# Performance work log

Hardware: AMD Instinct MI355X
Metric: run time of the kernel (lower is better)

Reference implementation:

```python
import jax, jax.numpy as jnp
import numpy as np

B, T, D, HD, HN, O = 32, 512, 512, 64, 16, 512
EPS = 1e-5


def setup_inputs() -> dict:
    key = jax.random.key(0)
    ks = jax.random.split(key, 12)
    s = lambda fan_in: 1.0 / np.sqrt(fan_in)
    inp = {
        "inputs": jax.random.normal(ks[0], (B, T, D), dtype=jnp.float32),
        "Wq": jax.random.uniform(ks[1], (HN, D, HD), jnp.float32, -s(D), s(D)),
        "bq": jnp.zeros((HN, HD), jnp.float32),
        "Wk": jax.random.uniform(ks[2], (HN, D, HD), jnp.float32, -s(D), s(D)),
        "bk": jnp.zeros((HN, HD), jnp.float32),
        "Wv": jax.random.uniform(ks[3], (HN, D, HD), jnp.float32, -s(D), s(D)),
        "bv": jnp.zeros((HN, HD), jnp.float32),
        "Wr": jax.random.uniform(ks[4], (D, O), jnp.float32, -s(D), s(D)),
        "br": jnp.zeros((O,), jnp.float32),
        "Wo": jax.random.uniform(ks[5], (HN * HD, O), jnp.float32, -s(HN * HD), s(HN * HD)),
        "bo": jnp.zeros((O,), jnp.float32),
        "ln1_w": jnp.ones((O,), jnp.float32),
        "ln1_b": jnp.zeros((O,), jnp.float32),
        "Wfc": jax.random.uniform(ks[6], (O, O), jnp.float32, -s(O), s(O)),
        "bfc": jnp.zeros((O,), jnp.float32),
        "ln2_w": jnp.ones((O,), jnp.float32),
        "ln2_b": jnp.zeros((O,), jnp.float32),
    }
    return inp


def _layernorm(x, w, b):
    mu = jnp.mean(x, axis=-1, keepdims=True)
    var = jnp.mean(jnp.square(x - mu), axis=-1, keepdims=True)
    return (x - mu) * jax.lax.rsqrt(var + EPS) * w + b


def reference(inputs, Wq, bq, Wk, bk, Wv, bv, Wr, br, Wo, bo,
              ln1_w, ln1_b, Wfc, bfc, ln2_w, ln2_b):
    # causal mask: multiply-then-subtract as in the original
    score_mask = jnp.tril(jnp.ones((T, T), jnp.float32))        # [T,T]
    padding_mask = (score_mask == 0).astype(jnp.float32) * 1e9  # [T,T]

    residual = inputs @ Wr + br                                  # [B,T,O]

    # batched per-head projections with nonstandard activations
    q = jax.nn.relu(jnp.einsum('btd,hdf->bhtf', inputs, Wq) + bq[None, :, None, :])
    k = jax.nn.relu(jnp.einsum('btd,hdf->bhtf', inputs, Wk) + bk[None, :, None, :])
    v = jnp.tanh(jnp.einsum('btd,hdf->bhtf', inputs, Wv) + bv[None, :, None, :])

    scores = jnp.einsum('bhtf,bhsf->bhts', q, k) / jnp.sqrt(jnp.float32(HD))
    scores = scores * score_mask - padding_mask                  # [B,H,T,T]
    weights = jax.nn.softmax(scores, axis=-1)
    heads = jnp.einsum('bhts,bhsf->bhtf', weights, v)            # [B,H,T,HD]

    # concat heads (head order preserved) + tanh output projection
    concat = heads.transpose(0, 2, 1, 3).reshape(B, T, HN * HD)
    out = jnp.tanh(concat @ Wo + bo)                             # [B,T,O]

    out = _layernorm(out + residual, ln1_w, ln1_b)
    fc = jax.nn.relu(out @ Wfc + bfc)
    out = _layernorm(fc + out, ln2_w, ln2_b)
    return out
```

## Files before the change

### kernel.cpp

```cpp
#include <hip/hip_runtime.h>
#include <hip/hip_bf16.h>

#define B_  32
#define T_  512
#define D_  512
#define HD_ 64
#define HN_ 16
#define O_  512
#define M_  (B_ * T_)
#define NQ_ (HN_ * HD_)

typedef __bf16 bf16;
typedef __attribute__((ext_vector_type(8))) __bf16 bf16x8;
typedef __attribute__((ext_vector_type(4))) __bf16 bf16x4;
typedef __attribute__((ext_vector_type(4))) float f32x4;

static __device__ __forceinline__ f32x4 mfma16(bf16x8 a, bf16x8 b, f32x4 c) {
    return __builtin_amdgcn_mfma_f32_16x16x32_bf16(a, b, c, 0, 0, 0);
}

static __device__ __forceinline__ void load_lds_16B(const bf16* g, bf16* l) {
    __builtin_amdgcn_global_load_lds(
        (const __attribute__((address_space(1))) unsigned int*)(unsigned long long)g,
        (__attribute__((address_space(3))) unsigned int*)(unsigned long long)l,
        16, 0, 0);
}

static __device__ __forceinline__ float fast_tanh(float x) {
    return 1.f - 2.f / (__expf(2.f * x) + 1.f);
}

static __device__ __forceinline__ int2 swz_block() {
    const int nx = gridDim.x;
    const int nwg = nx * gridDim.y;
    int l = blockIdx.y * nx + blockIdx.x;
    l = (l & 7) * (nwg >> 3) + (l >> 3);
    return make_int2(l % nx, l / nx);
}

__global__ __launch_bounds__(256) void prep_headw_kernel(
    const float* __restrict__ Wq, const float* __restrict__ Wk,
    const float* __restrict__ Wv, bf16* __restrict__ wall)
{
    __shared__ bf16 tl[64][72];
    int id = blockIdx.x;
    const int kt = id & 7; id >>= 3;
    const int h = id & 15; id >>= 4;
    const float* src = (id == 0) ? Wq : (id == 1) ? Wk : Wv;
    bf16* dst = wall + (size_t)id * (1024 * 512);
    const int tid = threadIdx.x;
    const int k0 = kt * 64;
#pragma unroll
    for (int i = 0; i < 4; i++) {
        const int e = i * 256 + tid;
        const int kk = e >> 4, f4 = (e & 15) * 4;
        const f32x4 v = *(const f32x4*)(src + ((size_t)h * 512 + k0 + kk) * 64 + f4);
#pragma unroll
        for (int j = 0; j < 4; j++) tl[f4 + j][kk] = (bf16)v[j];
    }
    __syncthreads();
#pragma unroll
    for (int i = 0; i < 2; i++) {
        const int e = i * 256 + tid;
        const int f = e >> 3, kc = (e & 7) * 8;
        *(bf16x8*)(dst + ((size_t)h * 64 + f) * 512 + k0 + kc) = *(const bf16x8*)&tl[f][kc];
    }
}

__global__ __launch_bounds__(256) void prep_plain_kernel(
    const float* __restrict__ Wr, const float* __restrict__ Wo,
    const float* __restrict__ Wfc,
    bf16* __restrict__ wrt, bf16* __restrict__ wot, bf16* __restrict__ wfct)
{
    __shared__ bf16 tl[64][72];
    int id = blockIdx.x;
    const float* src; bf16* dst; int K;
    if (id < 64)       { src = Wr;  dst = wrt;  K = 512;  }
    else if (id < 192) { src = Wo;  dst = wot;  K = 1024; id -= 64; }
    else               { src = Wfc; dst = wfct; K = 512;  id -= 192; }
    const int kt = id >> 3, nt = id & 7;
    const int k0 = kt * 64, n0 = nt * 64;
    const int tid = threadIdx.x;
#pragma unroll
    for (int i = 0; i < 4; i++) {
        const int e = i * 256 + tid;
        const int kk = e >> 4, n4 = (e & 15) * 4;
        const f32x4 v = *(const f32x4*)(src + (size_t)(k0 + kk) * 512 + n0 + n4);
#pragma unroll
        for (int j = 0; j < 4; j++) tl[n4 + j][kk] = (bf16)v[j];
    }
    __syncthreads();
#pragma unroll
    for (int i = 0; i < 2; i++) {
        const int e = i * 256 + tid;
        const int nn = e >> 3, kc = (e & 7) * 8;
        *(bf16x8*)(dst + (size_t)(n0 + nn) * K + k0 + kc) = *(const bf16x8*)&tl[nn][kc];
    }
}

__global__ __launch_bounds__(256) void conv_input_kernel(
    const float* __restrict__ in, bf16* __restrict__ out)
{
    const size_t i = ((size_t)blockIdx.x * 256 + threadIdx.x) * 8;
    f32x4 x0 = *(const f32x4*)(in + i);
    f32x4 x1 = *(const f32x4*)(in + i + 4);
    bf16x8 v;
    v[0] = (bf16)x0[0]; v[1] = (bf16)x0[1]; v[2] = (bf16)x0[2]; v[3] = (bf16)x0[3];
    v[4] = (bf16)x1[0]; v[5] = (bf16)x1[1]; v[6] = (bf16)x1[2]; v[7] = (bf16)x1[3];
    *(bf16x8*)(out + i) = v;
}

__global__ __launch_bounds__(256) void pack_bias_kernel(
    const float* __restrict__ bq, const float* __restrict__ bk,
    const float* __restrict__ bv, const float* __restrict__ br,
    float* __restrict__ ball)
{
    const int i = blockIdx.x * 256 + threadIdx.x;
    float v = (i < 1024) ? bq[i]
            : (i < 2048) ? bk[i - 1024]
            : (i < 3072) ? bv[i - 2048] : br[i - 3072];
    ball[i] = v;
}

__device__ __forceinline__ void gemm_mainloop_db(
    const bf16* __restrict__ A, const bf16* __restrict__ Wt,
    const int K, const int m0, const int n0, const int tid,
    bf16 (*As)[128 * 64], bf16 (*Bs)[128 * 64], f32x4 (&acc)[4][4])
{
    const int lane = tid & 63;
    const int w = tid >> 6;
    const int wr = w >> 1, wc = w & 1;
    const int lr = lane & 15, lg = lane >> 4;
    const int nt = K >> 6;

    auto STAGE = [&](int buf, int k0) {
#pragma unroll
        for (int i = 0; i < 4; i++) {
            const int p = i * 256 + tid;
            const int row = p >> 3;
            const int g = (p & 7) ^ (row & 7);
            load_lds_16B(A + (size_t)(m0 + row) * K + k0 + g * 8, As[buf] + p * 8);
            load_lds_16B(Wt + (size_t)(n0 + row) * K + k0 + g * 8, Bs[buf] + p * 8);
        }
    };

    STAGE(0, 0);
    asm volatile("s_waitcnt vmcnt(0)\n\ts_barrier" ::: "memory");

    for (int t = 0; t < nt; t++) {
        const int cur = t & 1;
        if (t + 1 < nt) STAGE(cur ^ 1, (t + 1) << 6);
#pragma unroll
        for (int kc = 0; kc < 2; kc++) {
            bf16x8 a[4], b[4];
#pragma unroll
            for (int mi = 0; mi < 4; mi++) {
                const int row = wr * 64 + mi * 16 + lr;
                a[mi] = *(const bf16x8*)&As[cur][row * 64 + ((((kc << 2) | lg) ^ (row & 7)) << 3)];
            }
#pragma unroll
            for (int nj = 0; nj < 4; nj++) {
                const int row = wc * 64 + nj * 16 + lr;
                b[nj] = *(const bf16x8*)&Bs[cur][row * 64 + ((((kc << 2) | lg) ^ (row & 7)) << 3)];
            }
#pragma unroll
            for (int mi = 0; mi < 4; mi++)
#pragma unroll
                for (int nj = 0; nj < 4; nj++)
                    acc[mi][nj] = mfma16(a[mi], b[nj], acc[mi][nj]);
        }
        asm volatile("s_waitcnt vmcnt(0)\n\ts_barrier" ::: "memory");
    }
}

__global__ __launch_bounds__(256) void gemm_qkvr_kernel(
    const bf16* __restrict__ A, const bf16* __restrict__ Wall,
    const float* __restrict__ ball,
    bf16* __restrict__ qc, bf16* __restrict__ kb, bf16* __restrict__ vt,
    bf16* __restrict__ resb)
{
    __shared__ bf16 As[2][128 * 64];
    __shared__ bf16 Bs[2][128 * 64];
    const int tid = threadIdx.x;
    const int2 bc = swz_block();
    const int m0 = bc.y * 128, n0 = bc.x * 128;
    f32x4 acc[4][4];
    const f32x4 zero4 = {0.f, 0.f, 0.f, 0.f};
#pragma unroll
    for (int i = 0; i < 4; i++)
#pragma unroll
        for (int j = 0; j < 4; j++) acc[i][j] = zero4;

    gemm_mainloop_db(A, Wall, 512, m0, n0, tid, As, Bs, acc);

    const int lane = tid & 63, w = tid >> 6;
    const int wr = w >> 1, wc = w & 1, lr = lane & 15, lg = lane >> 4;
    const int region = n0 >> 10;
#pragma unroll
    for (int mi = 0; mi < 4; mi++) {
#pragma unroll
        for (int nj = 0; nj < 4; nj++) {
            const int n = n0 + wc * 64 + nj * 16 + lr;
            const float bn = ball[n];
            if (region == 2) {
                const int m = m0 + wr * 64 + mi * 16 + lg * 4;
                const int bb = m >> 9, t = m & 511;
                const int nn = n - 2048, hh = nn >> 6, f = nn & 63;
                bf16x4 st;
#pragma unroll
                for (int r = 0; r < 4; r++) st[r] = (bf16)fast_tanh(acc[mi][nj][r] + bn);
                *(bf16x4*)(vt + (((size_t)(bb * 16 + hh) * 64 + f) << 9) + t) = st;
            } else if (region == 3) {
                const int nn = n - 3072;
#pragma unroll
                for (int r = 0; r < 4; r++) {
                    const int m = m0 + wr * 64 + mi * 16 + lg * 4 + r;
                    resb[(size_t)m * 512 + nn] = (bf16)(acc[mi][nj][r] + bn);
                }
            } else {
                bf16* dst = region ? kb : qc;
                const int nn = n & 1023;
#pragma unroll
                for (int r = 0; r < 4; r++) {
                    const int m = m0 + wr * 64 + mi * 16 + lg * 4 + r;
                    dst[(size_t)m * 1024 + nn] = (bf16)fmaxf(acc[mi][nj][r] + bn, 0.f);
                }
            }
        }
    }
}

template <int ACT>
__global__ __launch_bounds__(256) void gemm_std_kernel(
    const bf16* __restrict__ A, const bf16* __restrict__ Wt,
    const float* __restrict__ bias, bf16* __restrict__ C, const int K)
{
    __shared__ bf16 As[2][128 * 64];
    __shared__ bf16 Bs[2][128 * 64];
    const int tid = threadIdx.x;
    const int2 bc = swz_block();
    const int m0 = bc.y * 128, n0 = bc.x * 128;
    f32x4 acc[4][4];
    const f32x4 zero4 = {0.f, 0.f, 0.f, 0.f};
#pragma unroll
    for (int i = 0; i < 4; i++)
#pragma unroll
        for (int j = 0; j < 4; j++) acc[i][j] = zero4;

    gemm_mainloop_db(A, Wt, K, m0, n0, tid, As, Bs, acc);

    const int lane = tid & 63, w = tid >> 6;
    const int wr = w >> 1, wc = w & 1, lr = lane & 15, lg = lane >> 4;
#pragma unroll
    for (int mi = 0; mi < 4; mi++) {
#pragma unroll
        for (int nj = 0; nj < 4; nj++) {
            const int n = n0 + wc * 64 + nj * 16 + lr;
            const float bn = bias[n];
#pragma unroll
            for (int r = 0; r < 4; r++) {
                const int m = m0 + wr * 64 + mi * 16 + lg * 4 + r;
                float v = acc[mi][nj][r] + bn;
                if constexpr (ACT == 1) v = fmaxf(v, 0.f);
                else if constexpr (ACT == 2) v = fast_tanh(v);
                C[(size_t)m * 512 + n] = (bf16)v;
            }
        }
    }
}

static __device__ __forceinline__ int sigma_k(int t) {
    return (t & 32) | ((t & 4) << 2) | ((t & 24) >> 1) | (t & 3);
}

__global__ __launch_bounds__(256) void mfma_attn_kernel(
    const bf16* __restrict__ Kb, const bf16* __restrict__ Vt, bf16* __restrict__ QC)
{
    __shared__ bf16 Ks[2][64][72];
    __shared__ bf16 Vts[2][64][72];

    int l = blockIdx.x;
    l = (l & 7) * 256 + (l >> 3);
    const int qb = l & 3;
    const int h = (l >> 2) & 15;
    const int b = l >> 6;
    const int tid = threadIdx.x;
    const int lane = tid & 63;
    const int w = tid >> 6;
    const int lr = lane & 15, lg = lane >> 4;

    const int qrow0 = qb * 128 + w * 32;
    const size_t qbase = ((size_t)b * T_ + qrow0) * NQ_ + h * 64;
    const int bh = b * HN_ + h;

    bf16x8 qf[2][2];
#pragma unroll
    for (int mi = 0; mi < 2; mi++)
#pragma unroll
        for (int kc = 0; kc < 2; kc++)
            qf[mi][kc] = *(const bf16x8*)(QC + qbase + (size_t)(mi * 16 + lr) * NQ_ + kc * 32 + lg * 8);

    const f32x4 zero4 = {0.f, 0.f, 0.f, 0.f};
    f32x4 o[2][4];
    float m_st[2] = {-1e30f, -1e30f}, l_st[2] = {0.f, 0.f};
#pragma unroll
    for (int mi = 0; mi < 2; mi++)
#pragma unroll
        for (int dj = 0; dj < 4; dj++) o[mi][dj] = zero4;

    const int nsb = 2 * qb + 2;

    bf16x8 kreg[2], vreg[2];
    auto LOADR = [&](int sb) {
#pragma unroll
        for (int i = 0; i < 2; i++) {
            const int ci = i * 256 + tid, row = ci >> 3, cc = ci & 7;
            kreg[i] = *(const bf16x8*)(Kb + ((size_t)b * T_ + sb * 64 + row) * NQ_ + h * 64 + cc * 8);
            vreg[i] = *(const bf16x8*)(Vt + ((size_t)bh * 64 + row) * T_ + sb * 64 + cc * 8);
        }
    };
    auto WRITE = [&](int buf) {
#pragma unroll
        for (int i = 0; i < 2; i++) {
            const int ci = i * 256 + tid, row = ci >> 3, cc = ci & 7;
            *(bf16x8*)&Ks[buf][sigma_k(row)][cc * 8] = kreg[i];
            *(bf16x8*)&Vts[buf][row][cc * 8] = vreg[i];
        }
    };

    LOADR(0); WRITE(0); __syncthreads();
    int cur = 0;

    for (int sb = 0; sb < nsb; sb++) {
        const bool pf = (sb + 1 < nsb);
        if (pf) LOADR(sb + 1);

        if (sb * 64 <= qrow0 + 31) {
            f32x4 sc[2][4];
#pragma unroll
            for (int mi = 0; mi < 2; mi++)
#pragma unroll
                for (int nj = 0; nj < 4; nj++) sc[mi][nj] = zero4;
#pragma unroll
            for (int kc = 0; kc < 2; kc++) {
                bf16x8 kf[4];
#pragma unroll
                for (int nj = 0; nj < 4; nj++)
                    kf[nj] = *(const bf16x8*)&Ks[cur][nj * 16 + lr][kc * 32 + lg * 8];
#pragma unroll
                for (int mi = 0; mi < 2; mi++)
#pragma unroll
                    for (int nj = 0; nj < 4; nj++)
                        sc[mi][nj] = mfma16(kf[nj], qf[mi][kc], sc[mi][nj]);
            }
            const bool needmask = (sb * 64 + 63 > qrow0);
            float tm[2];
#pragma unroll
            for (int mi = 0; mi < 2; mi++) {
                const int qg = qrow0 + mi * 16 + lr;
                float mx = -1e30f;
#pragma unroll
                for (int nj = 0; nj < 4; nj++) {
                    const int kvb = sb * 64 + ((nj >> 1) << 5) + ((nj & 1) << 2) + lg * 8;
#pragma unroll
                    for (int r = 0; r < 4; r++) {
                        float s = sc[mi][nj][r] * 0.125f;
                        if (needmask && (kvb + r > qg)) s = -1e30f;
                        sc[mi][nj][r] = s;
                        mx = fmaxf(mx, s);
                    }
                }
                mx = fmaxf(mx, __shfl_xor(mx, 16));
                mx = fmaxf(mx, __shfl_xor(mx, 32));
                tm[mi] = mx;
            }
            const bool defer = (tm[0] <= m_st[0] + 8.f) && (tm[1] <= m_st[1] + 8.f);
            if (!__all(defer)) {
#pragma unroll
                for (int mi = 0; mi < 2; mi++) {
                    const float mn = fmaxf(m_st[mi], tm[mi]);
                    const float sf = __expf(m_st[mi] - mn);
                    m_st[mi] = mn;
                    l_st[mi] *= sf;
#pragma unroll
                    for (int dj = 0; dj < 4; dj++)
#pragma unroll
                        for (int r = 0; r < 4; r++) o[mi][dj][r] *= sf;
                }
            }
            bf16x4 pk[2][4];
#pragma unroll
            for (int mi = 0; mi < 2; mi++) {
                float ts = 0.f;
#pragma unroll
                for (int nj = 0; nj < 4; nj++)
#pragma unroll
                    for (int r = 0; r < 4; r++) {
                        const float p = __expf(sc[mi][nj][r] - m_st[mi]);
                        ts += p;
                        pk[mi][nj][r] = (bf16)p;
                    }
                ts += __shfl_xor(ts, 16);
                ts += __shfl_xor(ts, 32);
                l_st[mi] += ts;
            }
#pragma unroll
            for (int kc = 0; kc < 2; kc++) {
                bf16x8 vf[4], pf2[2];
#pragma unroll
                for (int mi = 0; mi < 2; mi++) {
                    bf16x8 t;
#pragma unroll
                    for (int r = 0; r < 4; r++) { t[r] = pk[mi][2 * kc][r]; t[r + 4] = pk[mi][2 * kc + 1][r]; }
                    pf2[mi] = t;
                }
#pragma unroll
                for (int dj = 0; dj < 4; dj++)
                    vf[dj] = *(const bf16x8*)&Vts[cur][dj * 16 + lr][kc * 32 + lg * 8];
#pragma unroll
                for (int mi = 0; mi < 2; mi++)
#pragma unroll
                    for (int dj = 0; dj < 4; dj++)
                        o[mi][dj] = mfma16(vf[dj], pf2[mi], o[mi][dj]);
            }
        }

        __syncthreads();
        if (pf) WRITE(cur ^ 1);
        __syncthreads();
        cur ^= 1;
    }

#pragma unroll
    for (int mi = 0; mi < 2; mi++) {
        const float inv = 1.f / l_st[mi];
        const size_t rowoff = qbase + (size_t)(mi * 16 + lr) * NQ_;
#pragma unroll
        for (int dj = 0; dj < 4; dj++) {
            bf16x4 st;
#pragma unroll
            for (int r = 0; r < 4; r++) st[r] = (bf16)(o[mi][dj][r] * inv);
            *(bf16x4*)(QC + rowoff + dj * 16 + lg * 4) = st;
        }
    }
}

template <bool F32OUT>
__global__ __launch_bounds__(256) void ln_kernel(
    const bf16* __restrict__ xa, const bf16* __restrict__ xb,
    const float* __restrict__ w, const float* __restrict__ bias,
    void* __restrict__ outv)
{
    const int row = blockIdx.x * 4 + (threadIdx.x >> 6);
    const int ln = threadIdx.x & 63;
    const size_t base = (size_t)row * 512 + ln * 8;
    const bf16x8 va = *(const bf16x8*)(xa + base);
    const bf16x8 vb = *(const bf16x8*)(xb + base);
    float x[8];
    float s = 0.f;
#pragma unroll
    for (int i = 0; i < 8; i++) { x[i] = (float)va[i] + (float)vb[i]; s += x[i]; }
#pragma unroll
    for (int off = 32; off >= 1; off >>= 1) s += __shfl_xor(s, off);
    const float mean = s * (1.f / 512.f);
    float ss = 0.f;
#pragma unroll
    for (int i = 0; i < 8; i++) { x[i] -= mean; ss += x[i] * x[i]; }
#pragma unroll
    for (int off = 32; off >= 1; off >>= 1) ss += __shfl_xor(ss, off);
    const float inv = rsqrtf(ss * (1.f / 512.f) + 1e-5f);
    const f32x4 w0 = *(const f32x4*)(w + ln * 8);
    const f32x4 w1 = *(const f32x4*)(w + ln * 8 + 4);
    const f32x4 b0 = *(const f32x4*)(bias + ln * 8);
    const f32x4 b1 = *(const f32x4*)(bias + ln * 8 + 4);
    if constexpr (F32OUT) {
        f32x4 y0, y1;
#pragma unroll
        for (int i = 0; i < 4; i++) {
            y0[i] = x[i] * inv * w0[i] + b0[i];
            y1[i] = x[4 + i] * inv * w1[i] + b1[i];
        }
        *(f32x4*)((float*)outv + base) = y0;
        *(f32x4*)((float*)outv + base + 4) = y1;
    } else {
        bf16x8 y;
#pragma unroll
        for (int i = 0; i < 4; i++) {
            y[i] = (bf16)(x[i] * inv * w0[i] + b0[i]);
            y[4 + i] = (bf16)(x[4 + i] * inv * w1[i] + b1[i]);
        }
        *(bf16x8*)((bf16*)outv + base) = y;
    }
}

extern "C" void kernel_launch(void* const* d_in, const int* in_sizes, int n_in,
                              void* d_out, int out_size, void* d_ws, size_t ws_size,
                              hipStream_t stream)
{
    const float* inputs = (const float*)d_in[0];
    const float* Wq = (const float*)d_in[1];
    const float* bq = (const float*)d_in[2];
    const float* Wk = (const float*)d_in[3];
    const float* bk = (const float*)d_in[4];
    const float* Wv = (const float*)d_in[5];
    const float* bv = (const float*)d_in[6];
    const float* Wr = (const float*)d_in[7];
    const float* br = (const float*)d_in[8];
    const float* Wo = (const float*)d_in[9];
    const float* bo = (const float*)d_in[10];
    const float* ln1w = (const float*)d_in[11];
    const float* ln1b = (const float*)d_in[12];
    const float* Wfc = (const float*)d_in[13];
    const float* bfc = (const float*)d_in[14];
    const float* ln2w = (const float*)d_in[15];
    const float* ln2b = (const float*)d_in[16];
    float* out = (float*)d_out;

    const size_t MB = 1024ull * 1024ull;
    char* ws = (char*)d_ws;
    bf16* qc   = (bf16*)(ws);
    bf16* kb   = (bf16*)(ws + 32 * MB);
    bf16* vt   = (bf16*)(ws + 64 * MB);
    bf16* xin  = (bf16*)(ws + 96 * MB);
    bf16* wall = (bf16*)(ws + 112 * MB);
    bf16* wot  = (bf16*)(ws + 112 * MB + 3670016);
    bf16* wfct = (bf16*)(ws + 112 * MB + 3670016 + 1048576);
    float* ball = (float*)(ws + 112 * MB + 3670016 + 1048576 + 524288);
    bf16* wrt  = wall + (size_t)3072 * 512;
    bf16* resb = (bf16*)d_out;
    bf16* att  = kb;
    bf16* ln1  = kb + (size_t)8 * MB;
    bf16* fcb  = vt;

    const dim3 blk(256);

    conv_input_kernel<<<dim3(4096), blk, 0, stream>>>(inputs, xin);
    prep_headw_kernel<<<dim3(384), blk, 0, stream>>>(Wq, Wk, Wv, wall);
    prep_plain_kernel<<<dim3(256), blk, 0, stream>>>(Wr, Wo, Wfc, wrt, wot, wfct);
    pack_bias_kernel<<<dim3(14), blk, 0, stream>>>(bq, bk, bv, br, ball);

    gemm_qkvr_kernel<<<dim3(28, 128), blk, 0, stream>>>(xin, wall, ball, qc, kb, vt, resb);
    mfma_attn_kernel<<<dim3(B_ * HN_ * 4), blk, 0, stream>>>(kb, vt, qc);
    gemm_std_kernel<2><<<dim3(4, 128), blk, 0, stream>>>(qc, wot, bo, att, 1024);
    ln_kernel<false><<<dim3(4096), blk, 0, stream>>>(att, resb, ln1w, ln1b, ln1);
    gemm_std_kernel<1><<<dim3(4, 128), blk, 0, stream>>>(ln1, wfct, bfc, fcb, 512);
    ln_kernel<true ><<<dim3(4096), blk, 0, stream>>>(fcb, ln1, ln2w, ln2b, out);
}
```

Baseline: 247.9 us.

## Use 4-stage K32 GEMM pipeline, LDS-staged epilogue stores, and MFMA priority hints

Replaces the double-buffered K=64 GEMM main loop with a four-buffer K=32 ring that keeps two tiles in flight and waits on partial vmcnt. The GEMM epilogues for Q, K, the residual and the standard GEMMs now go through LDS and are written back as 16-byte row stores instead of scattered 2-byte stores. The 1/8 score scale is folded into the Q projection epilogue. The attention kernel adds s_setprio around its MFMA blocks and drops one __syncthreads before the prefetch write. Together these aim to cut global-load latency stalls and uncoalesced epilogue traffic. The unswizzled K32 LDS layout may add bank conflicts, and removing the barrier risks a race on the attention buffers.

```diff
diff --git a/kernel.cpp b/kernel.cpp
--- a/kernel.cpp
+++ b/kernel.cpp
@@ -122,54 +122,97 @@
     ball[i] = v;
 }
 
-__device__ __forceinline__ void gemm_mainloop_db(
+__device__ __forceinline__ void gemm_mainloop_p4(
     const bf16* __restrict__ A, const bf16* __restrict__ Wt,
     const int K, const int m0, const int n0, const int tid,
-    bf16 (*As)[128 * 64], bf16 (*Bs)[128 * 64], f32x4 (&acc)[4][4])
+    bf16* SL, f32x4 (&acc)[4][4])
 {
     const int lane = tid & 63;
     const int w = tid >> 6;
     const int wr = w >> 1, wc = w & 1;
     const int lr = lane & 15, lg = lane >> 4;
-    const int nt = K >> 6;
-
-    auto STAGE = [&](int buf, int k0) {
-#pragma unroll
-        for (int i = 0; i < 4; i++) {
-            const int p = i * 256 + tid;
-            const int row = p >> 3;
-            const int g = (p & 7) ^ (row & 7);
-            load_lds_16B(A + (size_t)(m0 + row) * K + k0 + g * 8, As[buf] + p * 8);
-            load_lds_16B(Wt + (size_t)(n0 + row) * K + k0 + g * 8, Bs[buf] + p * 8);
-        }
+    const int nt = K >> 5;
+
+    const int p0 = tid, p1 = tid + 256;
+    const bf16* aS0 = A + (size_t)(m0 + (p0 >> 2)) * K + (p0 & 3) * 8;
+    const bf16* aS1 = A + (size_t)(m0 + (p1 >> 2)) * K + (p1 & 3) * 8;
+    const bf16* bS0 = Wt + (size_t)(n0 + (p0 >> 2)) * K + (p0 & 3) * 8;
+    const bf16* bS1 = Wt + (size_t)(n0 + (p1 >> 2)) * K + (p1 & 3) * 8;
+
+    auto STAGE = [&](int t) {
+        bf16* Ab = SL + (t & 3) * 4096;
+        bf16* Bb = SL + 16384 + (t & 3) * 4096;
+        const int k0 = t << 5;
+        load_lds_16B(aS0 + k0, Ab + p0 * 8);
+        load_lds_16B(aS1 + k0, Ab + p1 * 8);
+        load_lds_16B(bS0 + k0, Bb + p0 * 8);
+        load_lds_16B(bS1 + k0, Bb + p1 * 8);
     };
 
-    STAGE(0, 0);
-    asm volatile("s_waitcnt vmcnt(0)\n\ts_barrier" ::: "memory");
+    STAGE(0); STAGE(1);
+    asm volatile("s_waitcnt vmcnt(4)" ::: "memory");
+    __builtin_amdgcn_s_barrier();
 
     for (int t = 0; t < nt; t++) {
-        const int cur = t & 1;
-        if (t + 1 < nt) STAGE(cur ^ 1, (t + 1) << 6);
-#pragma unroll
-        for (int kc = 0; kc < 2; kc++) {
-            bf16x8 a[4], b[4];
-#pragma unroll
-            for (int mi = 0; mi < 4; mi++) {
-                const int row = wr * 64 + mi * 16 + lr;
-                a[mi] = *(const bf16x8*)&As[cur][row * 64 + ((((kc << 2) | lg) ^ (row & 7)) << 3)];
-            }
-#pragma unroll
-            for (int nj = 0; nj < 4; nj++) {
-                const int row = wc * 64 + nj * 16 + lr;
-                b[nj] = *(const bf16x8*)&Bs[cur][row * 64 + ((((kc << 2) | lg) ^ (row & 7)) << 3)];
-            }
-#pragma unroll
-            for (int mi = 0; mi < 4; mi++)
-#pragma unroll
-                for (int nj = 0; nj < 4; nj++)
-                    acc[mi][nj] = mfma16(a[mi], b[nj], acc[mi][nj]);
-        }
-        asm volatile("s_waitcnt vmcnt(0)\n\ts_barrier" ::: "memory");
+        if (t + 2 < nt) {
+            STAGE(t + 2);
+            asm volatile("s_waitcnt vmcnt(4)" ::: "memory");
+        } else {
+            asm volatile("s_waitcnt vmcnt(0)" ::: "memory");
+        }
+        __builtin_amdgcn_s_barrier();
+        const bf16* Ab = SL + (t & 3) * 4096;
+        const bf16* Bb = SL + 16384 + (t & 3) * 4096;
+        bf16x8 a[4], b[4];
+#pragma unroll
+        for (int mi = 0; mi < 4; mi++)
+            a[mi] = *(const bf16x8*)&Ab[(wr * 64 + mi * 16 + lr) * 32 + lg * 8];
+#pragma unroll
+        for (int nj = 0; nj < 4; nj++)
+            b[nj] = *(const bf16x8*)&Bb[(wc * 64 + nj * 16 + lr) * 32 + lg * 8];
+        __builtin_amdgcn_s_setprio(1);
+#pragma unroll
+        for (int mi = 0; mi < 4; mi++)
+#pragma unroll
+            for (int nj = 0; nj < 4; nj++)
+                acc[mi][nj] = mfma16(a[mi], b[nj], acc[mi][nj]);
+        __builtin_amdgcn_s_setprio(0);
+    }
+    __builtin_amdgcn_s_barrier();
+}
+
+template <int ACT>
+__device__ __forceinline__ void epi_transpose_store(
+    f32x4 (&acc)[4][4], const float* __restrict__ ball, bf16* SL,
+    bf16* __restrict__ dst, const int pitch, const int m0, const int nglob0,
+    const int nb, const float scale, const int tid)
+{
+    const int lane = tid & 63, w = tid >> 6;
+    const int wr = w >> 1, wc = w & 1, lr = lane & 15, lg = lane >> 4;
+#pragma unroll
+    for (int mi = 0; mi < 4; mi++) {
+#pragma unroll
+        for (int nj = 0; nj < 4; nj++) {
+            const float bn = ball[nglob0 + wc * 64 + nj * 16 + lr];
+            const int rbase = wr * 64 + mi * 16 + lg * 4;
+            const int cidx = wc * 64 + nj * 16 + lr;
+#pragma unroll
+            for (int r = 0; r < 4; r++) {
+                float v = acc[mi][nj][r] + bn;
+                if constexpr (ACT == 1) v = fmaxf(v, 0.f);
+                SL[(rbase + r) * 136 + cidx] = (bf16)(v * scale);
+            }
+        }
+    }
+    __syncthreads();
+#pragma unroll
+    for (int pass = 0; pass < 4; pass++) {
+        const int rr = pass * 32 + (tid >> 3);
+        const int cc = (tid & 7) * 16;
+        bf16x8 v0 = *(const bf16x8*)&SL[rr * 136 + cc];
+        bf16x8 v1 = *(const bf16x8*)&SL[rr * 136 + cc + 8];
+        *(bf16x8*)(dst + (size_t)(m0 + rr) * pitch + nb + cc) = v0;
+        *(bf16x8*)(dst + (size_t)(m0 + rr) * pitch + nb + cc + 8) = v1;
     }
 }
 
@@ -179,8 +222,7 @@
     bf16* __restrict__ qc, bf16* __restrict__ kb, bf16* __restrict__ vt,
     bf16* __restrict__ resb)
 {
-    __shared__ bf16 As[2][128 * 64];
-    __shared__ bf16 Bs[2][128 * 64];
+    __shared__ bf16 SL[32768];
     const int tid = threadIdx.x;
     const int2 bc = swz_block();
     const int m0 = bc.y * 128, n0 = bc.x * 128;
@@ -191,18 +233,24 @@
 #pragma unroll
         for (int j = 0; j < 4; j++) acc[i][j] = zero4;
 
-    gemm_mainloop_db(A, Wall, 512, m0, n0, tid, As, Bs, acc);
-
-    const int lane = tid & 63, w = tid >> 6;
-    const int wr = w >> 1, wc = w & 1, lr = lane & 15, lg = lane >> 4;
+    gemm_mainloop_p4(A, Wall, 512, m0, n0, tid, SL, acc);
+
     const int region = n0 >> 10;
-#pragma unroll
-    for (int mi = 0; mi < 4; mi++) {
-#pragma unroll
-        for (int nj = 0; nj < 4; nj++) {
-            const int n = n0 + wc * 64 + nj * 16 + lr;
-            const float bn = ball[n];
-            if (region == 2) {
+    if (region == 0) {
+        epi_transpose_store<1>(acc, ball, SL, qc, 1024, m0, n0, n0 & 1023, 0.125f, tid);
+    } else if (region == 1) {
+        epi_transpose_store<1>(acc, ball, SL, kb, 1024, m0, n0, n0 & 1023, 1.f, tid);
+    } else if (region == 3) {
+        epi_transpose_store<0>(acc, ball, SL, resb, 512, m0, n0, n0 - 3072, 1.f, tid);
+    } else {
+        const int lane = tid & 63, w = tid >> 6;
+        const int wr = w >> 1, wc = w & 1, lr = lane & 15, lg = lane >> 4;
+#pragma unroll
+        for (int mi = 0; mi < 4; mi++) {
+#pragma unroll
+            for (int nj = 0; nj < 4; nj++) {
+                const int n = n0 + wc * 64 + nj * 16 + lr;
+                const float bn = ball[n];
                 const int m = m0 + wr * 64 + mi * 16 + lg * 4;
                 const int bb = m >> 9, t = m & 511;
                 const int nn = n - 2048, hh = nn >> 6, f = nn & 63;
@@ -210,21 +258,6 @@
 #pragma unroll
                 for (int r = 0; r < 4; r++) st[r] = (bf16)fast_tanh(acc[mi][nj][r] + bn);
                 *(bf16x4*)(vt + (((size_t)(bb * 16 + hh) * 64 + f) << 9) + t) = st;
-            } else if (region == 3) {
-                const int nn = n - 3072;
-#pragma unroll
-                for (int r = 0; r < 4; r++) {
-                    const int m = m0 + wr * 64 + mi * 16 + lg * 4 + r;
-                    resb[(size_t)m * 512 + nn] = (bf16)(acc[mi][nj][r] + bn);
-                }
-            } else {
-                bf16* dst = region ? kb : qc;
-                const int nn = n & 1023;
-#pragma unroll
-                for (int r = 0; r < 4; r++) {
-                    const int m = m0 + wr * 64 + mi * 16 + lg * 4 + r;
-                    dst[(size_t)m * 1024 + nn] = (bf16)fmaxf(acc[mi][nj][r] + bn, 0.f);
-                }
             }
         }
     }
@@ -235,8 +268,7 @@
     const bf16* __restrict__ A, const bf16* __restrict__ Wt,
     const float* __restrict__ bias, bf16* __restrict__ C, const int K)
 {
-    __shared__ bf16 As[2][128 * 64];
-    __shared__ bf16 Bs[2][128 * 64];
+    __shared__ bf16 SL[32768];
     const int tid = threadIdx.x;
     const int2 bc = swz_block();
     const int m0 = bc.y * 128, n0 = bc.x * 128;
@@ -247,7 +279,7 @@
 #pragma unroll
         for (int j = 0; j < 4; j++) acc[i][j] = zero4;
 
-    gemm_mainloop_db(A, Wt, K, m0, n0, tid, As, Bs, acc);
+    gemm_mainloop_p4(A, Wt, K, m0, n0, tid, SL, acc);
 
     const int lane = tid & 63, w = tid >> 6;
     const int wr = w >> 1, wc = w & 1, lr = lane & 15, lg = lane >> 4;
@@ -255,17 +287,27 @@
     for (int mi = 0; mi < 4; mi++) {
 #pragma unroll
         for (int nj = 0; nj < 4; nj++) {
-            const int n = n0 + wc * 64 + nj * 16 + lr;
-            const float bn = bias[n];
+            const float bn = bias[n0 + wc * 64 + nj * 16 + lr];
+            const int rbase = wr * 64 + mi * 16 + lg * 4;
+            const int cidx = wc * 64 + nj * 16 + lr;
 #pragma unroll
             for (int r = 0; r < 4; r++) {
-                const int m = m0 + wr * 64 + mi * 16 + lg * 4 + r;
                 float v = acc[mi][nj][r] + bn;
                 if constexpr (ACT == 1) v = fmaxf(v, 0.f);
                 else if constexpr (ACT == 2) v = fast_tanh(v);
-                C[(size_t)m * 512 + n] = (bf16)v;
-            }
-        }
+                SL[(rbase + r) * 136 + cidx] = (bf16)v;
+            }
+        }
+    }
+    __syncthreads();
+#pragma unroll
+    for (int pass = 0; pass < 4; pass++) {
+        const int rr = pass * 32 + (tid >> 3);
+        const int cc = (tid & 7) * 16;
+        bf16x8 v0 = *(const bf16x8*)&SL[rr * 136 + cc];
+        bf16x8 v1 = *(const bf16x8*)&SL[rr * 136 + cc + 8];
+        *(bf16x8*)(C + (size_t)(m0 + rr) * 512 + n0 + cc) = v0;
+        *(bf16x8*)(C + (size_t)(m0 + rr) * 512 + n0 + cc + 8) = v1;
     }
 }
 
@@ -341,6 +383,7 @@
             for (int mi = 0; mi < 2; mi++)
 #pragma unroll
                 for (int nj = 0; nj < 4; nj++) sc[mi][nj] = zero4;
+            __builtin_amdgcn_s_setprio(1);
 #pragma unroll
             for (int kc = 0; kc < 2; kc++) {
                 bf16x8 kf[4];
@@ -353,6 +396,7 @@
                     for (int nj = 0; nj < 4; nj++)
                         sc[mi][nj] = mfma16(kf[nj], qf[mi][kc], sc[mi][nj]);
             }
+            __builtin_amdgcn_s_setprio(0);
             const bool needmask = (sb * 64 + 63 > qrow0);
             float tm[2];
 #pragma unroll
@@ -364,7 +408,7 @@
                     const int kvb = sb * 64 + ((nj >> 1) << 5) + ((nj & 1) << 2) + lg * 8;
 #pragma unroll
                     for (int r = 0; r < 4; r++) {
-                        float s = sc[mi][nj][r] * 0.125f;
+                        float s = sc[mi][nj][r];
                         if (needmask && (kvb + r > qg)) s = -1e30f;
                         sc[mi][nj][r] = s;
                         mx = fmaxf(mx, s);
@@ -404,6 +448,7 @@
                 ts += __shfl_xor(ts, 32);
                 l_st[mi] += ts;
             }
+            __builtin_amdgcn_s_setprio(1);
 #pragma unroll
             for (int kc = 0; kc < 2; kc++) {
                 bf16x8 vf[4], pf2[2];
@@ -423,9 +468,9 @@
                     for (int dj = 0; dj < 4; dj++)
                         o[mi][dj] = mfma16(vf[dj], pf2[mi], o[mi][dj]);
             }
-        }
-
-        __syncthreads();
+            __builtin_amdgcn_s_setprio(0);
+        }
+
         if (pf) WRITE(cur ^ 1);
         __syncthreads();
         cur ^= 1;
```

Result: no change. 252.6 us (+1.9%).
